# Kernel optimization log

Hardware: AMD Instinct MI355X
Metric: run time of the kernel (lower is better)

The kernel has to match this reference:

```python
import jax, jax.numpy as jnp
import numpy as np


def _chamfer(x1, x2):
    """Squared-L2 chamfer distances.
    x1: [B,N,3], x2: [B,M,3]
    returns dist1: [B,N] (min over x2), dist2: [B,M] (min over x1).
    """
    sq1 = jnp.sum(x1 * x1, axis=-1)           # [B,N]
    sq2 = jnp.sum(x2 * x2, axis=-1)           # [B,M]
    cross = jnp.einsum('bnd,bmd->bnm', x1, x2)  # [B,N,M]
    d = sq1[:, :, None] + sq2[:, None, :] - 2.0 * cross
    dist1 = jnp.min(d, axis=2)
    dist2 = jnp.min(d, axis=1)
    return dist1, dist2


def setup_inputs() -> dict:
    key = jax.random.key(0)
    k1, k2, k3 = jax.random.split(key, 3)
    partial = jax.random.normal(k1, (4, 2048, 3), dtype=jnp.float32)
    infer = jax.random.normal(k2, (4, 8192, 3), dtype=jnp.float32)
    complete = jax.random.normal(k3, (4, 8192, 3), dtype=jnp.float32)
    return {"partial": partial, "infer": infer, "complete": complete}


def reference(partial, infer, complete):
    # dist_cp: per-complete-point min sq-dist to partial
    _, dist_cp = _chamfer(partial, complete)
    # dist_ic: per-infer-point min sq-dist to complete; dist_ci: per-complete min to infer
    dist_ic, dist_ci = _chamfer(infer, complete)
    max_dist_cp = jnp.max(dist_cp)
    weighted_dist_ci = dist_cp * dist_ci / max_dist_cp
    return jnp.mean(dist_ic) + jnp.mean(weighted_dist_ci)
```

## Files before the change

kernel.cpp:

```cpp
#include <hip/hip_runtime.h>


#define BATCH 4
#define NP    2048
#define NQ    8192
#define NTOT  (BATCH*NQ)
#define ONEB  0x3F80u

typedef float v16f __attribute__((ext_vector_type(16)));
typedef short v8s  __attribute__((ext_vector_type(8)));
union U4S8 { uint4 u; v8s s; };

__device__ __forceinline__ unsigned int bfr(float f) {
    unsigned int u = __float_as_uint(f);
    u += 0x7FFFu + ((u >> 16) & 1u);
    return (u >> 16);
}
__device__ __forceinline__ float bff(unsigned int h) {
    return __uint_as_float(h << 16);
}

__device__ __forceinline__ v8s buildA32(const float* qp, int half) {
    float qx = qp[0], qy = qp[1], qz = qp[2];
    unsigned xh = bfr(qx), yh = bfr(qy), zh = bfr(qz);
    unsigned xl = bfr(qx - bff(xh)), yl = bfr(qy - bff(yh)), zl = bfr(qz - bff(zh));
    float s = fmaf(qx, qx, fmaf(qy, qy, qz*qz));
    unsigned sh = bfr(s), sl = bfr(s - bff(sh));
    unsigned mxh = bfr(-2.0f*bff(xh)), myh = bfr(-2.0f*bff(yh)), mzh = bfr(-2.0f*bff(zh));
    unsigned mxl = bfr(-2.0f*bff(xl)), myl = bfr(-2.0f*bff(yl)), mzl = bfr(-2.0f*bff(zl));
    uint4 q0 = make_uint4(mxh | (myh<<16), mzh | (mxh<<16), myh | (mzh<<16), mxl | (myl<<16));
    uint4 q1 = make_uint4(mzl | (ONEB<<16), ONEB | (sh<<16), sl, 0u);
    U4S8 r;
    r.u.x = half ? q1.x : q0.x;
    r.u.y = half ? q1.y : q0.y;
    r.u.z = half ? q1.z : q0.z;
    r.u.w = half ? q1.w : q0.w;
    return r.s;
}

#define R16(M) M(0) M(1) M(2) M(3) M(4) M(5) M(6) M(7) \
               M(8) M(9) M(10) M(11) M(12) M(13) M(14) M(15)
#define WR(r) { int rw = ((r) & 3) + 8*((r) >> 2) + 4*half; \
                red[rw*33 + n] = mnA[r]; red[1056 + rw*33 + n] = mnB[r]; }

__global__ __launch_bounds__(256, 4) void minDistKernel(
    const float* __restrict__ partial,
    const float* __restrict__ infer,
    const float* __restrict__ complete,
    unsigned int* __restrict__ keys)
{
    __shared__ __align__(16) unsigned char lds[33792];

    const int tid = threadIdx.x;
    const int lane = tid & 63, w = tid >> 6;
    const int half = lane >> 5, n = lane & 31;

    const int x = blockIdx.x, z = blockIdx.z;
    int cid, task;
    if (z < 2)       { task = 0; cid = z; }
    else if (z < 10) { task = 1; cid = z - 2; }
    else             { task = 2; cid = z - 10; }
    const int b = x >> 5;

    const float* qraw; const float* craw; int trow;
    if (task == 0)      { qraw = complete + b*NQ*3; craw = partial  + (b*NP + cid*1024)*3; trow = 0; }
    else if (task == 1) { qraw = infer    + b*NQ*3; craw = complete + (b*NQ + cid*1024)*3; trow = 1; }
    else                { qraw = complete + b*NQ*3; craw = infer    + (b*NQ + cid*1024)*3; trow = 2; }

    {
        const float4* p4 = (const float4*)(craw) + tid*3;
        float4 f0 = p4[0], f1 = p4[1], f2 = p4[2];
        float cs[12] = {f0.x,f0.y,f0.z,f0.w, f1.x,f1.y,f1.z,f1.w, f2.x,f2.y,f2.z,f2.w};
        #pragma unroll
        for (int r = 0; r < 4; ++r) {
            float cx = cs[r*3+0], cy = cs[r*3+1], cz = cs[r*3+2];
            unsigned xh = bfr(cx), yh = bfr(cy), zh = bfr(cz);
            unsigned xl = bfr(cx - bff(xh)), yl = bfr(cy - bff(yh)), zl = bfr(cz - bff(zh));
            float s = fmaf(cx, cx, fmaf(cy, cy, cz*cz));
            unsigned sh = bfr(s), sl = bfr(s - bff(sh));
            int c = tid*4 + r, t = c >> 5, cn = c & 31;
            *(uint4*)(lds + t*1024 + cn*16) =
                make_uint4(xh | (yh<<16), zh | (xl<<16), yl | (zl<<16), xh | (yh<<16));
            *(uint4*)(lds + t*1024 + 512 + cn*16) =
                make_uint4(zh | (sh<<16), sl | (ONEB<<16), ONEB, 0u);
        }
    }

    const int q0 = (x & 31)*256 + w*64;
    v8s a0 = buildA32(qraw + (q0 + n)*3, half);
    v8s a1 = buildA32(qraw + (q0 + 32 + n)*3, half);

    const float INF = __builtin_inff();
    v16f mnA, mnB, Z;
    #pragma unroll
    for (int r = 0; r < 16; ++r) { mnA[r] = INF; mnB[r] = INF; Z[r] = 0.0f; }

    __syncthreads();

    #pragma unroll 1
    for (int t = 0; t < 32; t += 2) {
        U4S8 b0u, b1u;
        b0u.u = *(const uint4*)(lds + t*1024 + lane*16);
        b1u.u = *(const uint4*)(lds + (t+1)*1024 + lane*16);
        v8s bf0 = b0u.s, bf1 = b1u.s;
        {
            v16f d0 = __builtin_amdgcn_mfma_f32_32x32x16_bf16(a0, bf0, Z, 0, 0, 0);
            v16f d1 = __builtin_amdgcn_mfma_f32_32x32x16_bf16(a0, bf1, Z, 0, 0, 0);
            #pragma unroll
            for (int r = 0; r < 16; ++r) mnA[r] = fminf(mnA[r], fminf(d0[r], d1[r]));
        }
        {
            v16f d0 = __builtin_amdgcn_mfma_f32_32x32x16_bf16(a1, bf0, Z, 0, 0, 0);
            v16f d1 = __builtin_amdgcn_mfma_f32_32x32x16_bf16(a1, bf1, Z, 0, 0, 0);
            #pragma unroll
            for (int r = 0; r < 16; ++r) mnB[r] = fminf(mnB[r], fminf(d0[r], d1[r]));
        }
    }

    __syncthreads();
    float* red = (float*)lds + w*2112;
    R16(WR)
    __syncthreads();

    const float* myrow = red + half*1056 + n*33;
    float p0 = myrow[0], p1 = myrow[1], p2 = myrow[2], p3 = myrow[3];
    #pragma unroll
    for (int j = 4; j < 32; j += 4) {
        p0 = fminf(p0, myrow[j+0]); p1 = fminf(p1, myrow[j+1]);
        p2 = fminf(p2, myrow[j+2]); p3 = fminf(p3, myrow[j+3]);
    }
    float m = fminf(fminf(p0, p1), fminf(p2, p3));

    unsigned int* krow = keys + trow*NTOT + b*NQ;
    atomicMin(&krow[q0 + half*32 + n], __float_as_uint(fmaxf(m, 0.0f)));
}

__global__ __launch_bounds__(1024) void reduceKernel(
    const unsigned int* __restrict__ keys, float* __restrict__ out)
{
    const int tid = threadIdx.x;
    const uint4* kcp = (const uint4*)(keys);
    const uint4* kic = (const uint4*)(keys + NTOT);
    const uint4* kci = (const uint4*)(keys + 2*NTOT);

    float mx = 0.0f, s1 = 0.0f, s2 = 0.0f;
    #pragma unroll
    for (int k = 0; k < NTOT/4/1024; ++k) {
        int i = k*1024 + tid;
        uint4 a = kcp[i]; uint4 bb = kic[i]; uint4 c = kci[i];
        float a0 = __uint_as_float(a.x),  a1 = __uint_as_float(a.y);
        float a2 = __uint_as_float(a.z),  a3 = __uint_as_float(a.w);
        mx = fmaxf(mx, fmaxf(fmaxf(a0, a1), fmaxf(a2, a3)));
        s1 += (__uint_as_float(bb.x) + __uint_as_float(bb.y))
            + (__uint_as_float(bb.z) + __uint_as_float(bb.w));
        s2 = fmaf(a0, __uint_as_float(c.x), fmaf(a1, __uint_as_float(c.y),
             fmaf(a2, __uint_as_float(c.z), fmaf(a3, __uint_as_float(c.w), s2))));
    }

    #pragma unroll
    for (int off = 32; off > 0; off >>= 1) {
        mx = fmaxf(mx, __shfl_down(mx, off));
        s1 += __shfl_down(s1, off);
        s2 += __shfl_down(s2, off);
    }

    __shared__ float smx[16], ss1[16], ss2[16];
    const int wid = tid >> 6, lane = tid & 63;
    if (lane == 0) { smx[wid] = mx; ss1[wid] = s1; ss2[wid] = s2; }
    __syncthreads();

    if (tid == 0) {
        float M = smx[0], S1 = ss1[0], S2 = ss2[0];
        for (int i = 1; i < 16; ++i) { M = fmaxf(M, smx[i]); S1 += ss1[i]; S2 += ss2[i]; }
        out[0] = S1 / (float)NTOT + S2 / (M * (float)NTOT);
    }
}

extern "C" void kernel_launch(void* const* d_in, const int* in_sizes, int n_in,
                              void* d_out, int out_size, void* d_ws, size_t ws_size,
                              hipStream_t stream) {
    const float* partial  = (const float*)d_in[0];
    const float* infer    = (const float*)d_in[1];
    const float* complete = (const float*)d_in[2];
    unsigned int* keys = (unsigned int*)d_ws;

    minDistKernel<<<dim3(128, 1, 18), 256, 0, stream>>>(partial, infer, complete, keys);
    reduceKernel<<<1, 1024, 0, stream>>>(keys, (float*)d_out);
}
```

Measured before the change: 82.66 us.

## Precompute bf16 split operand packing in a separate kernel and stream B from global

A new pack kernel converts every point once into its hi/lo bf16 MFMA operand layout and writes it to workspace. Before, each block redid this conversion for its query and candidate points. The distance kernel now loads the packed A fragments directly and reads B tiles from global memory with a one-step register prefetch, replacing LDS staging and the barrier before the loop. This costs an extra kernel launch and a workspace round trip, and the B reads now depend on L2/global latency instead of LDS.

```diff
diff --git a/kernel.cpp b/kernel.cpp
--- a/kernel.cpp
+++ b/kernel.cpp
@@ -7,6 +7,13 @@
 #define NTOT  (BATCH*NQ)
 #define ONEB  0x3F80u
 
+#define KEYS_BYTES (3*NTOT*4)
+#define AC_OFF  KEYS_BYTES
+#define AI_OFF  (AC_OFF + BATCH*NQ*32)
+#define BP_OFF  (AI_OFF + BATCH*NQ*32)
+#define BC_OFF  (BP_OFF + BATCH*NP*32)
+#define BI_OFF  (BC_OFF + BATCH*NQ*32)
+
 typedef float v16f __attribute__((ext_vector_type(16)));
 typedef short v8s  __attribute__((ext_vector_type(8)));
 union U4S8 { uint4 u; v8s s; };
@@ -20,22 +27,50 @@
     return __uint_as_float(h << 16);
 }
 
-__device__ __forceinline__ v8s buildA32(const float* qp, int half) {
-    float qx = qp[0], qy = qp[1], qz = qp[2];
-    unsigned xh = bfr(qx), yh = bfr(qy), zh = bfr(qz);
-    unsigned xl = bfr(qx - bff(xh)), yl = bfr(qy - bff(yh)), zl = bfr(qz - bff(zh));
-    float s = fmaf(qx, qx, fmaf(qy, qy, qz*qz));
-    unsigned sh = bfr(s), sl = bfr(s - bff(sh));
-    unsigned mxh = bfr(-2.0f*bff(xh)), myh = bfr(-2.0f*bff(yh)), mzh = bfr(-2.0f*bff(zh));
-    unsigned mxl = bfr(-2.0f*bff(xl)), myl = bfr(-2.0f*bff(yl)), mzl = bfr(-2.0f*bff(zl));
-    uint4 q0 = make_uint4(mxh | (myh<<16), mzh | (mxh<<16), myh | (mzh<<16), mxl | (myl<<16));
-    uint4 q1 = make_uint4(mzl | (ONEB<<16), ONEB | (sh<<16), sl, 0u);
-    U4S8 r;
-    r.u.x = half ? q1.x : q0.x;
-    r.u.y = half ? q1.y : q0.y;
-    r.u.z = half ? q1.z : q0.z;
-    r.u.w = half ? q1.w : q0.w;
-    return r.s;
+__global__ __launch_bounds__(256) void packKernel(
+    const float* __restrict__ partial,
+    const float* __restrict__ infer,
+    const float* __restrict__ complete,
+    unsigned char* __restrict__ ws)
+{
+    const int idx = blockIdx.x * 256 + threadIdx.x;
+    const float* pt;
+    unsigned char* bbase;
+    unsigned char* abase = nullptr;
+    int c;
+    if (idx < 8192) {
+        int b = idx >> 11; c = idx & 2047;
+        pt = partial + idx*3;
+        bbase = ws + BP_OFF + (b*2)*32768;
+    } else if (idx < 40960) {
+        int li = idx - 8192; int b = li >> 13; c = li & 8191;
+        pt = complete + li*3;
+        bbase = ws + BC_OFF + (b*8)*32768;
+        abase = ws + AC_OFF + (b*NQ + c)*32;
+    } else {
+        int li = idx - 40960; int b = li >> 13; c = li & 8191;
+        pt = infer + li*3;
+        bbase = ws + BI_OFF + (b*8)*32768;
+        abase = ws + AI_OFF + (b*NQ + c)*32;
+    }
+
+    const float x = pt[0], y = pt[1], z = pt[2];
+    const unsigned xh = bfr(x), yh = bfr(y), zh = bfr(z);
+    const unsigned xl = bfr(x - bff(xh)), yl = bfr(y - bff(yh)), zl = bfr(z - bff(zh));
+    const float s = fmaf(x, x, fmaf(y, y, z*z));
+    const unsigned sh = bfr(s), sl = bfr(s - bff(sh));
+
+    const int chunk = c >> 10, cc = c & 1023, t = cc >> 5, cn = cc & 31;
+    unsigned char* bdst = bbase + chunk*32768 + t*1024 + cn*16;
+    *(uint4*)(bdst)       = make_uint4(xh | (yh<<16), zh | (xl<<16), yl | (zl<<16), xh | (yh<<16));
+    *(uint4*)(bdst + 512) = make_uint4(zh | (sh<<16), sl | (ONEB<<16), ONEB, 0u);
+
+    if (abase) {
+        const unsigned mxh = bfr(-2.0f*bff(xh)), myh = bfr(-2.0f*bff(yh)), mzh = bfr(-2.0f*bff(zh));
+        const unsigned mxl = bfr(-2.0f*bff(xl)), myl = bfr(-2.0f*bff(yl)), mzl = bfr(-2.0f*bff(zl));
+        *(uint4*)(abase)      = make_uint4(mxh | (myh<<16), mzh | (mxh<<16), myh | (mzh<<16), mxl | (myl<<16));
+        *(uint4*)(abase + 16) = make_uint4(mzl | (ONEB<<16), ONEB | (sh<<16), sl, 0u);
+    }
 }
 
 #define R16(M) M(0) M(1) M(2) M(3) M(4) M(5) M(6) M(7) \
@@ -44,12 +79,10 @@
                 red[rw*33 + n] = mnA[r]; red[1056 + rw*33 + n] = mnB[r]; }
 
 __global__ __launch_bounds__(256, 4) void minDistKernel(
-    const float* __restrict__ partial,
-    const float* __restrict__ infer,
-    const float* __restrict__ complete,
+    const unsigned char* __restrict__ ws,
     unsigned int* __restrict__ keys)
 {
-    __shared__ __align__(16) unsigned char lds[33792];
+    __shared__ float red_s[4*2112];
 
     const int tid = threadIdx.x;
     const int lane = tid & 63, w = tid >> 6;
@@ -62,63 +95,48 @@
     else             { task = 2; cid = z - 10; }
     const int b = x >> 5;
 
-    const float* qraw; const float* craw; int trow;
-    if (task == 0)      { qraw = complete + b*NQ*3; craw = partial  + (b*NP + cid*1024)*3; trow = 0; }
-    else if (task == 1) { qraw = infer    + b*NQ*3; craw = complete + (b*NQ + cid*1024)*3; trow = 1; }
-    else                { qraw = complete + b*NQ*3; craw = infer    + (b*NQ + cid*1024)*3; trow = 2; }
-
-    {
-        const float4* p4 = (const float4*)(craw) + tid*3;
-        float4 f0 = p4[0], f1 = p4[1], f2 = p4[2];
-        float cs[12] = {f0.x,f0.y,f0.z,f0.w, f1.x,f1.y,f1.z,f1.w, f2.x,f2.y,f2.z,f2.w};
-        #pragma unroll
-        for (int r = 0; r < 4; ++r) {
-            float cx = cs[r*3+0], cy = cs[r*3+1], cz = cs[r*3+2];
-            unsigned xh = bfr(cx), yh = bfr(cy), zh = bfr(cz);
-            unsigned xl = bfr(cx - bff(xh)), yl = bfr(cy - bff(yh)), zl = bfr(cz - bff(zh));
-            float s = fmaf(cx, cx, fmaf(cy, cy, cz*cz));
-            unsigned sh = bfr(s), sl = bfr(s - bff(sh));
-            int c = tid*4 + r, t = c >> 5, cn = c & 31;
-            *(uint4*)(lds + t*1024 + cn*16) =
-                make_uint4(xh | (yh<<16), zh | (xl<<16), yl | (zl<<16), xh | (yh<<16));
-            *(uint4*)(lds + t*1024 + 512 + cn*16) =
-                make_uint4(zh | (sh<<16), sl | (ONEB<<16), ONEB, 0u);
-        }
-    }
+    const unsigned char* aArr; const unsigned char* bArr; int trow;
+    if (task == 0)      { aArr = ws + AC_OFF + b*NQ*32; bArr = ws + BP_OFF + (b*2 + cid)*32768; trow = 0; }
+    else if (task == 1) { aArr = ws + AI_OFF + b*NQ*32; bArr = ws + BC_OFF + (b*8 + cid)*32768; trow = 1; }
+    else                { aArr = ws + AC_OFF + b*NQ*32; bArr = ws + BI_OFF + (b*8 + cid)*32768; trow = 2; }
 
     const int q0 = (x & 31)*256 + w*64;
-    v8s a0 = buildA32(qraw + (q0 + n)*3, half);
-    v8s a1 = buildA32(qraw + (q0 + 32 + n)*3, half);
+    U4S8 a0u, a1u;
+    a0u.u = *(const uint4*)(aArr + (((q0 + n)*2 + half) << 4));
+    a1u.u = *(const uint4*)(aArr + (((q0 + 32 + n)*2 + half) << 4));
+
+    const uint4* bp = (const uint4*)bArr;
+    uint4 c0 = bp[lane], c1 = bp[64 + lane];
 
     const float INF = __builtin_inff();
     v16f mnA, mnB, Z;
     #pragma unroll
     for (int r = 0; r < 16; ++r) { mnA[r] = INF; mnB[r] = INF; Z[r] = 0.0f; }
 
-    __syncthreads();
-
     #pragma unroll 1
     for (int t = 0; t < 32; t += 2) {
-        U4S8 b0u, b1u;
-        b0u.u = *(const uint4*)(lds + t*1024 + lane*16);
-        b1u.u = *(const uint4*)(lds + (t+1)*1024 + lane*16);
+        int tn = t + 2; if (tn >= 32) tn = 30;
+        uint4 n0 = bp[tn*64 + lane];
+        uint4 n1 = bp[tn*64 + 64 + lane];
+
+        U4S8 b0u, b1u; b0u.u = c0; b1u.u = c1;
         v8s bf0 = b0u.s, bf1 = b1u.s;
         {
-            v16f d0 = __builtin_amdgcn_mfma_f32_32x32x16_bf16(a0, bf0, Z, 0, 0, 0);
-            v16f d1 = __builtin_amdgcn_mfma_f32_32x32x16_bf16(a0, bf1, Z, 0, 0, 0);
+            v16f d0 = __builtin_amdgcn_mfma_f32_32x32x16_bf16(a0u.s, bf0, Z, 0, 0, 0);
+            v16f d1 = __builtin_amdgcn_mfma_f32_32x32x16_bf16(a0u.s, bf1, Z, 0, 0, 0);
             #pragma unroll
             for (int r = 0; r < 16; ++r) mnA[r] = fminf(mnA[r], fminf(d0[r], d1[r]));
         }
         {
-            v16f d0 = __builtin_amdgcn_mfma_f32_32x32x16_bf16(a1, bf0, Z, 0, 0, 0);
-            v16f d1 = __builtin_amdgcn_mfma_f32_32x32x16_bf16(a1, bf1, Z, 0, 0, 0);
+            v16f d0 = __builtin_amdgcn_mfma_f32_32x32x16_bf16(a1u.s, bf0, Z, 0, 0, 0);
+            v16f d1 = __builtin_amdgcn_mfma_f32_32x32x16_bf16(a1u.s, bf1, Z, 0, 0, 0);
             #pragma unroll
             for (int r = 0; r < 16; ++r) mnB[r] = fminf(mnB[r], fminf(d0[r], d1[r]));
         }
-    }
-
-    __syncthreads();
-    float* red = (float*)lds + w*2112;
+        c0 = n0; c1 = n1;
+    }
+
+    float* red = red_s + w*2112;
     R16(WR)
     __syncthreads();
 
@@ -182,8 +200,10 @@
     const float* partial  = (const float*)d_in[0];
     const float* infer    = (const float*)d_in[1];
     const float* complete = (const float*)d_in[2];
+    unsigned char* ws  = (unsigned char*)d_ws;
     unsigned int* keys = (unsigned int*)d_ws;
 
-    minDistKernel<<<dim3(128, 1, 18), 256, 0, stream>>>(partial, infer, complete, keys);
+    packKernel<<<288, 256, 0, stream>>>(partial, infer, complete, ws);
+    minDistKernel<<<dim3(128, 1, 18), 256, 0, stream>>>(ws, keys);
     reduceKernel<<<1, 1024, 0, stream>>>(keys, (float*)d_out);
 }
```

Result: slower. 88.28 us (+6.8%).

## Spread final reduction over 32 blocks and prefetch next LDS tiles

Applied to the files above, without the earlier changes.

The single-block reduce kernel becomes 32 blocks of 256 threads. They combine partial max and sums through global atomics, and the last block to arrive writes the result. The min-distance loop now loads the next pair of B fragments from LDS before issuing the current MFMAs, to hide LDS latency. The scratch counters are zeroed inside the first kernel. The keys buffer is still never reset to infinity before the atomicMin calls, and the scratch zeroing relies on kernel ordering.

```diff
diff --git a/kernel.cpp b/kernel.cpp
--- a/kernel.cpp
+++ b/kernel.cpp
@@ -38,8 +38,8 @@
     return r.s;
 }
 
-#define R16(M) M(0) M(1) M(2) M(3) M(4) M(5) M(6) M(7) \
-               M(8) M(9) M(10) M(11) M(12) M(13) M(14) M(15)
+#define R16M(M) M(0) M(1) M(2) M(3) M(4) M(5) M(6) M(7) \
+                M(8) M(9) M(10) M(11) M(12) M(13) M(14) M(15)
 #define WR(r) { int rw = ((r) & 3) + 8*((r) >> 2) + 4*half; \
                 red[rw*33 + n] = mnA[r]; red[1056 + rw*33 + n] = mnB[r]; }
 
@@ -56,6 +56,14 @@
     const int half = lane >> 5, n = lane & 31;
 
     const int x = blockIdx.x, z = blockIdx.z;
+
+    if (x == 0 && z == 0 && tid == 0) {
+        keys[3*NTOT + 0] = 0u;
+        keys[3*NTOT + 1] = 0u;
+        keys[3*NTOT + 2] = 0u;
+        keys[3*NTOT + 3] = 0u;
+    }
+
     int cid, task;
     if (z < 2)       { task = 0; cid = z; }
     else if (z < 10) { task = 1; cid = z - 2; }
@@ -97,12 +105,17 @@
 
     __syncthreads();
 
+    U4S8 c0u, c1u;
+    c0u.u = *(const uint4*)(lds + 0*1024 + lane*16);
+    c1u.u = *(const uint4*)(lds + 1*1024 + lane*16);
     #pragma unroll 1
     for (int t = 0; t < 32; t += 2) {
-        U4S8 b0u, b1u;
-        b0u.u = *(const uint4*)(lds + t*1024 + lane*16);
-        b1u.u = *(const uint4*)(lds + (t+1)*1024 + lane*16);
-        v8s bf0 = b0u.s, bf1 = b1u.s;
+        const int tn = (t + 2) & 31;
+        U4S8 n0u, n1u;
+        n0u.u = *(const uint4*)(lds + tn*1024 + lane*16);
+        n1u.u = *(const uint4*)(lds + (tn+1)*1024 + lane*16);
+
+        v8s bf0 = c0u.s, bf1 = c1u.s;
         {
             v16f d0 = __builtin_amdgcn_mfma_f32_32x32x16_bf16(a0, bf0, Z, 0, 0, 0);
             v16f d1 = __builtin_amdgcn_mfma_f32_32x32x16_bf16(a0, bf1, Z, 0, 0, 0);
@@ -115,11 +128,12 @@
             #pragma unroll
             for (int r = 0; r < 16; ++r) mnB[r] = fminf(mnB[r], fminf(d0[r], d1[r]));
         }
+        c0u = n0u; c1u = n1u;
     }
 
     __syncthreads();
     float* red = (float*)lds + w*2112;
-    R16(WR)
+    R16M(WR)
     __syncthreads();
 
     const float* myrow = red + half*1056 + n*33;
@@ -135,27 +149,24 @@
     atomicMin(&krow[q0 + half*32 + n], __float_as_uint(fmaxf(m, 0.0f)));
 }
 
-__global__ __launch_bounds__(1024) void reduceKernel(
-    const unsigned int* __restrict__ keys, float* __restrict__ out)
+__global__ __launch_bounds__(256) void reduceKernel(
+    unsigned int* __restrict__ keys, float* __restrict__ out)
 {
     const int tid = threadIdx.x;
+    const int i = blockIdx.x * 256 + tid;
     const uint4* kcp = (const uint4*)(keys);
     const uint4* kic = (const uint4*)(keys + NTOT);
     const uint4* kci = (const uint4*)(keys + 2*NTOT);
-
-    float mx = 0.0f, s1 = 0.0f, s2 = 0.0f;
-    #pragma unroll
-    for (int k = 0; k < NTOT/4/1024; ++k) {
-        int i = k*1024 + tid;
-        uint4 a = kcp[i]; uint4 bb = kic[i]; uint4 c = kci[i];
-        float a0 = __uint_as_float(a.x),  a1 = __uint_as_float(a.y);
-        float a2 = __uint_as_float(a.z),  a3 = __uint_as_float(a.w);
-        mx = fmaxf(mx, fmaxf(fmaxf(a0, a1), fmaxf(a2, a3)));
-        s1 += (__uint_as_float(bb.x) + __uint_as_float(bb.y))
-            + (__uint_as_float(bb.z) + __uint_as_float(bb.w));
-        s2 = fmaf(a0, __uint_as_float(c.x), fmaf(a1, __uint_as_float(c.y),
-             fmaf(a2, __uint_as_float(c.z), fmaf(a3, __uint_as_float(c.w), s2))));
-    }
+    unsigned int* scr = keys + 3*NTOT;
+
+    uint4 a = kcp[i]; uint4 bb = kic[i]; uint4 c = kci[i];
+    float a0 = __uint_as_float(a.x),  a1 = __uint_as_float(a.y);
+    float a2 = __uint_as_float(a.z),  a3 = __uint_as_float(a.w);
+    float mx = fmaxf(fmaxf(a0, a1), fmaxf(a2, a3));
+    float s1 = (__uint_as_float(bb.x) + __uint_as_float(bb.y))
+             + (__uint_as_float(bb.z) + __uint_as_float(bb.w));
+    float s2 = fmaf(a0, __uint_as_float(c.x), fmaf(a1, __uint_as_float(c.y),
+               fmaf(a2, __uint_as_float(c.z), a3 * __uint_as_float(c.w))));
 
     #pragma unroll
     for (int off = 32; off > 0; off >>= 1) {
@@ -164,15 +175,26 @@
         s2 += __shfl_down(s2, off);
     }
 
-    __shared__ float smx[16], ss1[16], ss2[16];
+    __shared__ float smx[4], ss1[4], ss2[4];
     const int wid = tid >> 6, lane = tid & 63;
     if (lane == 0) { smx[wid] = mx; ss1[wid] = s1; ss2[wid] = s2; }
     __syncthreads();
 
     if (tid == 0) {
-        float M = smx[0], S1 = ss1[0], S2 = ss2[0];
-        for (int i = 1; i < 16; ++i) { M = fmaxf(M, smx[i]); S1 += ss1[i]; S2 += ss2[i]; }
-        out[0] = S1 / (float)NTOT + S2 / (M * (float)NTOT);
+        float M = fmaxf(fmaxf(smx[0], smx[1]), fmaxf(smx[2], smx[3]));
+        float S1 = (ss1[0] + ss1[1]) + (ss1[2] + ss1[3]);
+        float S2 = (ss2[0] + ss2[1]) + (ss2[2] + ss2[3]);
+        atomicMax(&scr[1], __float_as_uint(M));
+        atomicAdd((float*)&scr[2], S1);
+        atomicAdd((float*)&scr[3], S2);
+        __threadfence();
+        unsigned old = atomicAdd(&scr[0], 1u);
+        if (old == 31u) {
+            float Mt  = __uint_as_float(atomicOr(&scr[1], 0u));
+            float S1t = atomicAdd((float*)&scr[2], 0.0f);
+            float S2t = atomicAdd((float*)&scr[3], 0.0f);
+            out[0] = S1t / (float)NTOT + S2t / (Mt * (float)NTOT);
+        }
     }
 }
 
@@ -185,5 +207,5 @@
     unsigned int* keys = (unsigned int*)d_ws;
 
     minDistKernel<<<dim3(128, 1, 18), 256, 0, stream>>>(partial, infer, complete, keys);
-    reduceKernel<<<1, 1024, 0, stream>>>(keys, (float*)d_out);
-}
+    reduceKernel<<<32, 256, 0, stream>>>(keys, (float*)d_out);
+}
```

New measurement: 82.79 us. About the same (+0.2%).
